# Kernel optimization log

Hardware: AMD Instinct MI355X
Metric: run time of the kernel (lower is better)

The kernel has to match this reference:

```python
import jax, jax.numpy as jnp
import numpy as np

B, D, LD, LP = 8, 192, 128, 1024
FC = [1024, 1024, 512]
NC = 2


def setup_inputs() -> dict:
    key = jax.random.key(0)
    ks = jax.random.split(key, 18)
    s = 0.05  # small init scale for numerical sanity
    inp = {
        "drug_conv": jax.random.normal(ks[0], (B, D, LD), jnp.float32),
        "protein_conv": jax.random.normal(ks[1], (B, D, LP), jnp.float32),
        "Wd": jax.random.normal(ks[2], (D, D), jnp.float32) * s,
        "bd": jax.random.normal(ks[3], (D,), jnp.float32) * s,
        "Wp": jax.random.normal(ks[4], (D, D), jnp.float32) * s,
        "bp": jax.random.normal(ks[5], (D,), jnp.float32) * s,
        "Wa": jax.random.normal(ks[6], (D, D), jnp.float32) * s,
        "ba": jax.random.normal(ks[7], (D,), jnp.float32) * s,
        "W1": jax.random.normal(ks[8], (FC[0], 2 * D), jnp.float32) * s,
        "b1": jax.random.normal(ks[9], (FC[0],), jnp.float32) * s,
        "W2": jax.random.normal(ks[10], (FC[1], FC[0]), jnp.float32) * s,
        "b2": jax.random.normal(ks[11], (FC[1],), jnp.float32) * s,
        "W3": jax.random.normal(ks[12], (FC[2], FC[1]), jnp.float32) * s,
        "b3": jax.random.normal(ks[13], (FC[2],), jnp.float32) * s,
        "Wo": jax.random.normal(ks[14], (NC, FC[2]), jnp.float32) * s,
        "bo": jax.random.normal(ks[15], (NC,), jnp.float32) * s,
    }
    return inp


def reference(drug_conv, protein_conv, Wd, bd, Wp, bp, Wa, ba,
              W1, b1, W2, b2, W3, b3, Wo, bo):
    # drug_conv: (B, D, Ld); protein_conv: (B, D, Lp). Torch Linear: y = x @ W.T + b
    d_att = jnp.einsum('bdl,ed->ble', drug_conv, Wd) + bd      # (B, Ld, D)
    p_att = jnp.einsum('bdl,ed->ble', protein_conv, Wp) + bp   # (B, Lp, D)
    # broadcast additive cross-attention: (B, Ld, Lp, D)
    h = jax.nn.relu(d_att[:, :, None, :] + p_att[:, None, :, :])
    A = jnp.einsum('blpd,ed->blpe', h, Wa) + ba                # (B, Ld, Lp, D)
    comp_att = jax.nn.sigmoid(jnp.mean(A, axis=2))             # (B, Ld, D)
    prot_att = jax.nn.sigmoid(jnp.mean(A, axis=1))             # (B, Lp, D)
    # gated residual: x*0.5 + x*att  (att permuted back to (B, D, L))
    drug = drug_conv * (0.5 + jnp.transpose(comp_att, (0, 2, 1)))
    prot = protein_conv * (0.5 + jnp.transpose(prot_att, (0, 2, 1)))
    # MaxPool1d over full sequence length == max along last axis
    drug_pooled = jnp.max(drug, axis=2)                        # (B, D)
    prot_pooled = jnp.max(prot, axis=2)                        # (B, D)
    pair = jnp.concatenate([drug_pooled, prot_pooled], axis=1) # (B, 2D)
    lrelu = lambda x: jax.nn.leaky_relu(x, 0.01)
    h1 = lrelu(pair @ W1.T + b1)
    h2 = lrelu(h1 @ W2.T + b2)
    h3 = lrelu(h2 @ W3.T + b3)
    return h3 @ Wo.T + bo                                      # (B, num_classes)
```

## Files before the change

### kernel.cpp

```cpp
#include <hip/hip_runtime.h>
#include <math.h>

#define BB 8
#define DD 192
#define LLD 128
#define LLP 1024
#define FC1 1024
#define FC2 1024
#define FC3 512
#define NCLS 2
#define LT 16

__global__ void proj_both_kernel(const float* __restrict__ drug,
                                 const float* __restrict__ prot,
                                 const float* __restrict__ Wd,
                                 const float* __restrict__ bdv,
                                 const float* __restrict__ Wp,
                                 const float* __restrict__ bpv,
                                 float* __restrict__ d_att,
                                 float* __restrict__ p_att) {
    int blk = blockIdx.x;
    const float *x, *W, *bias;
    float* y;
    int L, b, l0;
    if (blk < BB * (LLD / LT)) {
        x = drug; W = Wd; bias = bdv; y = d_att; L = LLD;
        b = blk >> 3; l0 = (blk & 7) * LT;
    } else {
        int idx = blk - BB * (LLD / LT);
        x = prot; W = Wp; bias = bpv; y = p_att; L = LLP;
        b = idx >> 6; l0 = (idx & 63) * LT;
    }
    int tid = threadIdx.x;

    __shared__ float xs[LT][DD + 4];

    const float* xbase = x + (size_t)b * DD * L + l0;
#pragma unroll
    for (int k = 0; k < LT; ++k) {
        int idx = tid + k * DD;
        int d = idx >> 4;
        int j = idx & (LT - 1);
        xs[j][d] = xbase[(size_t)d * L + j];
    }
    __syncthreads();

    const int e = tid;
    const float be = bias[e];
    float acc[LT];
#pragma unroll
    for (int j = 0; j < LT; ++j) acc[j] = be;

    const float4* Wr4 = (const float4*)(W + (size_t)e * DD);
#pragma unroll 2
    for (int d4 = 0; d4 < DD / 4; ++d4) {
        float4 w = Wr4[d4];
#pragma unroll
        for (int j = 0; j < LT; ++j) {
            float4 h = *(const float4*)&xs[j][d4 * 4];
            acc[j] = fmaf(h.x, w.x, acc[j]);
            acc[j] = fmaf(h.y, w.y, acc[j]);
            acc[j] = fmaf(h.z, w.z, acc[j]);
            acc[j] = fmaf(h.w, w.w, acc[j]);
        }
    }

    float* ybase = y + ((size_t)b * L + l0) * DD;
#pragma unroll
    for (int j = 0; j < LT; ++j)
        ybase[(size_t)j * DD + e] = acc[j];
}

__global__ void cross_sort_kernel(const float* __restrict__ da,
                                  const float* __restrict__ pa,
                                  float* __restrict__ Hd_t,
                                  float* __restrict__ Hp_t) {
    int blk = blockIdx.x;
    int b = blk / (DD / 2);
    int dp = blk - b * (DD / 2);
    int d0 = dp * 2;
    int tid = threadIdx.x;

    __shared__ float skey[2][LLD];
    __shared__ int   sidx[2][LLD];
    __shared__ float sufs[2][LLD + 1];
    __shared__ int   cnt[2][LLD + 1];
    __shared__ float val[2][LLD + 1];

    {
        int a = tid >> 7, l = tid & 127;
        skey[a][l] = da[((size_t)b * LLD + l) * DD + d0 + a];
        sidx[a][l] = l;
    }
    for (int i = tid; i < 2 * (LLD + 1); i += 256) {
        int a = i / (LLD + 1), k = i - a * (LLD + 1);
        cnt[a][k] = 0;
        val[a][k] = 0.f;
    }
    __syncthreads();

    {
        int a = tid >> 7, i = tid & 127;
        for (int k = 2; k <= LLD; k <<= 1) {
            for (int j = k >> 1; j > 0; j >>= 1) {
                int ixj = i ^ j;
                if (ixj > i) {
                    float ki = skey[a][i], kj = skey[a][ixj];
                    bool up = ((i & k) == 0);
                    if ((ki > kj) == up) {
                        skey[a][i] = kj; skey[a][ixj] = ki;
                        int t = sidx[a][i]; sidx[a][i] = sidx[a][ixj]; sidx[a][ixj] = t;
                    }
                }
                __syncthreads();
            }
        }
    }

    if (tid < 2) {
        float s = 0.f;
        sufs[tid][LLD] = 0.f;
        for (int r = LLD - 1; r >= 0; --r) {
            s += skey[tid][r];
            sufs[tid][r] = s;
        }
    }
    __syncthreads();

    {
        int d_i = tid & 1, prow = tid >> 1;
        float* hprow = Hp_t + ((size_t)b * DD + d0 + d_i) * LLP;
        const float* qbase = pa + (size_t)b * LLP * DD + d0 + d_i;
#pragma unroll
        for (int batch = 0; batch < LLP / 128; ++batch) {
            int p = batch * 128 + prow;
            float q = qbase[(size_t)p * DD];
            float nq = -q;
            int pos = 0;
#pragma unroll
            for (int st = LLD; st > 0; st >>= 1) {
                int np = pos + st;
                if (np <= LLD && skey[d_i][np - 1] <= nq) pos = np;
            }
            hprow[p] = ((float)(LLD - pos) * q + sufs[d_i][pos]) * (1.0f / LLD);
            atomicAdd(&cnt[d_i][pos], 1);
            atomicAdd(&val[d_i][pos], q);
        }
    }
    __syncthreads();

    if (tid < 2) {
        int c = 0; float v = 0.f;
        for (int k = 0; k < LLD; ++k) {
            c += cnt[tid][k]; cnt[tid][k] = c;
            v += val[tid][k]; val[tid][k] = v;
        }
    }
    __syncthreads();

    {
        int a = tid >> 7, r = tid & 127;
        float hv = (skey[a][r] * (float)cnt[a][r] + val[a][r]) * (1.0f / LLP);
        Hd_t[((size_t)b * DD + d0 + a) * LLD + sidx[a][r]] = hv;
    }
}

__global__ void gemm_sig_both_kernel(const float* __restrict__ Hd_t,
                                     const float* __restrict__ Hp_t,
                                     const float* __restrict__ Wa,
                                     const float* __restrict__ ba,
                                     float* __restrict__ catt_t,
                                     float* __restrict__ psig_t) {
    int blk = blockIdx.x;
    const float* Ht;
    float* out_t;
    int L, b, l0;
    if (blk < BB * (LLD / LT)) {
        b = blk >> 3; l0 = (blk & 7) * LT;
        Ht = Hd_t; out_t = catt_t; L = LLD;
    } else {
        int idx = blk - BB * (LLD / LT);
        b = idx >> 6; l0 = (idx & 63) * LT;
        Ht = Hp_t; out_t = psig_t; L = LLP;
    }
    int tid = threadIdx.x;

    __shared__ float hs[LT][DD];
    __shared__ float cs[LT][DD + 1];

    const float* hrow = Ht + ((size_t)b * DD + tid) * L + l0;
#pragma unroll
    for (int j = 0; j < LT; ++j) hs[j][tid] = hrow[j];
    __syncthreads();

    const int e = tid;
    const float bias = ba[e];
    float acc[LT];
#pragma unroll
    for (int j = 0; j < LT; ++j) acc[j] = bias;

    const float4* Wr4 = (const float4*)(Wa + (size_t)e * DD);
#pragma unroll 2
    for (int d4 = 0; d4 < DD / 4; ++d4) {
        float4 w = Wr4[d4];
#pragma unroll
        for (int j = 0; j < LT; ++j) {
            float4 h = *(const float4*)&hs[j][d4 * 4];
            acc[j] = fmaf(h.x, w.x, acc[j]);
            acc[j] = fmaf(h.y, w.y, acc[j]);
            acc[j] = fmaf(h.z, w.z, acc[j]);
            acc[j] = fmaf(h.w, w.w, acc[j]);
        }
    }

#pragma unroll
    for (int j = 0; j < LT; ++j)
        cs[j][e] = 1.0f / (1.0f + __expf(-acc[j]));
    __syncthreads();

    float* obase = out_t + (size_t)b * DD * L + l0;
    for (int k = tid; k < LT * DD; k += DD) {
        int eo = k >> 4;
        int j = k & (LT - 1);
        obase[(size_t)eo * L + j] = cs[j][eo];
    }
}

__global__ void pool_pair_kernel(const float* __restrict__ drug,
                                 const float* __restrict__ prot,
                                 const float* __restrict__ catt_t,
                                 const float* __restrict__ psig_t,
                                 float* __restrict__ pair) {
    int bd = blockIdx.x;
    int b = bd / DD;
    int d = bd - b * DD;
    int lane = threadIdx.x;

    const float* dr = drug + (size_t)bd * LLD;
    const float* ca = catt_t + (size_t)bd * LLD;
    float m1 = -INFINITY;
#pragma unroll
    for (int k = 0; k < LLD / 64; ++k) {
        int l = lane + 64 * k;
        m1 = fmaxf(m1, dr[l] * (0.5f + ca[l]));
    }

    const float* pr = prot + (size_t)bd * LLP;
    const float* ps = psig_t + (size_t)bd * LLP;
    float m2 = -INFINITY;
#pragma unroll
    for (int k = 0; k < LLP / 64; ++k) {
        int p = lane + 64 * k;
        m2 = fmaxf(m2, pr[p] * (0.5f + ps[p]));
    }

#pragma unroll
    for (int off = 32; off > 0; off >>= 1) {
        m1 = fmaxf(m1, __shfl_xor(m1, off));
        m2 = fmaxf(m2, __shfl_xor(m2, off));
    }
    if (lane == 0) {
        pair[b * 2 * DD + d] = m1;
        pair[b * 2 * DD + DD + d] = m2;
    }
}

__global__ void fc_wave_kernel(const float* __restrict__ x,
                               const float* __restrict__ W,
                               const float* __restrict__ bias,
                               float* __restrict__ y,
                               int K, int N, int leaky) {
    int gtid = blockIdx.x * blockDim.x + threadIdx.x;
    int wid = gtid >> 6;
    int lane = gtid & 63;
    if (wid >= BB * N) return;
    int b = wid / N;
    int j = wid - b * N;
    const float4* xr = (const float4*)(x + (size_t)b * K);
    const float4* Wr = (const float4*)(W + (size_t)j * K);
    int K4 = K >> 2;
    float s = 0.f;
    for (int k = lane; k < K4; k += 64) {
        float4 xv = xr[k];
        float4 wv = Wr[k];
        s = fmaf(xv.x, wv.x, s);
        s = fmaf(xv.y, wv.y, s);
        s = fmaf(xv.z, wv.z, s);
        s = fmaf(xv.w, wv.w, s);
    }
#pragma unroll
    for (int off = 32; off > 0; off >>= 1) s += __shfl_xor(s, off);
    if (lane == 0) {
        float acc = s + bias[j];
        if (leaky) acc = (acc > 0.f) ? acc : 0.01f * acc;
        y[wid] = acc;
    }
}

extern "C" void kernel_launch(void* const* d_in, const int* in_sizes, int n_in,
                              void* d_out, int out_size, void* d_ws, size_t ws_size,
                              hipStream_t stream) {
    const float* drug = (const float*)d_in[0];
    const float* prot = (const float*)d_in[1];
    const float* Wd = (const float*)d_in[2];
    const float* bd = (const float*)d_in[3];
    const float* Wp = (const float*)d_in[4];
    const float* bp = (const float*)d_in[5];
    const float* Wa = (const float*)d_in[6];
    const float* ba = (const float*)d_in[7];
    const float* W1 = (const float*)d_in[8];
    const float* b1 = (const float*)d_in[9];
    const float* W2 = (const float*)d_in[10];
    const float* b2 = (const float*)d_in[11];
    const float* W3 = (const float*)d_in[12];
    const float* b3 = (const float*)d_in[13];
    const float* Wo = (const float*)d_in[14];
    const float* bo = (const float*)d_in[15];
    float* out = (float*)d_out;

    float* ws = (float*)d_ws;
    const size_t n_datt = (size_t)BB * LLD * DD;
    const size_t n_patt = (size_t)BB * LLP * DD;
    float* d_att  = ws;
    float* p_att  = d_att + n_datt;
    float* Hd_t   = p_att + n_patt;
    float* Hp_t   = Hd_t + n_datt;
    float* catt_t = Hp_t + n_patt;
    float* psig_t = catt_t + n_datt;
    float* pair   = psig_t + n_patt;
    float* h1     = pair + (size_t)BB * 2 * DD;
    float* h2     = h1 + (size_t)BB * FC1;
    float* h3     = h2 + (size_t)BB * FC2;

    proj_both_kernel<<<BB * (LLD / LT) + BB * (LLP / LT), DD, 0, stream>>>(
        drug, prot, Wd, bd, Wp, bp, d_att, p_att);

    cross_sort_kernel<<<BB * (DD / 2), 256, 0, stream>>>(d_att, p_att, Hd_t, Hp_t);

    gemm_sig_both_kernel<<<BB * (LLD / LT) + BB * (LLP / LT), DD, 0, stream>>>(
        Hd_t, Hp_t, Wa, ba, catt_t, psig_t);

    pool_pair_kernel<<<BB * DD, 64, 0, stream>>>(drug, prot, catt_t, psig_t, pair);

    fc_wave_kernel<<<(BB * FC1 * 64) / 256, 256, 0, stream>>>(pair, W1, b1, h1, 2 * DD, FC1, 1);
    fc_wave_kernel<<<(BB * FC2 * 64) / 256, 256, 0, stream>>>(h1, W2, b2, h2, FC1, FC2, 1);
    fc_wave_kernel<<<(BB * FC3 * 64) / 256, 256, 0, stream>>>(h2, W3, b3, h3, FC2, FC3, 1);
    fc_wave_kernel<<<(BB * NCLS * 64 + 255) / 256, 256, 0, stream>>>(h3, Wo, bo, out, FC3, NCLS, 0);
}
```

Baseline: 110.0 us.

## Use 4x4 register tiles in projection GEMMs and parallel scans in sort kernel

Measured after the change: 153.3 us. +39.3%, slower.

```diff
diff --git a/kernel.cpp b/kernel.cpp
--- a/kernel.cpp
+++ b/kernel.cpp
@@ -45,30 +45,45 @@
     }
     __syncthreads();
 
-    const int e = tid;
-    const float be = bias[e];
-    float acc[LT];
-#pragma unroll
-    for (int j = 0; j < LT; ++j) acc[j] = be;
-
-    const float4* Wr4 = (const float4*)(W + (size_t)e * DD);
+    int et = tid % 48;
+    int lg = tid / 48;
+    int e0 = et * 4;
+    int jl0 = lg * 4;
+
+    float acc[4][4];
+#pragma unroll
+    for (int i = 0; i < 4; ++i) {
+        float be = bias[e0 + i];
+#pragma unroll
+        for (int j = 0; j < 4; ++j) acc[i][j] = be;
+    }
+
+    const float4* W4 = (const float4*)W;
 #pragma unroll 2
     for (int d4 = 0; d4 < DD / 4; ++d4) {
-        float4 w = Wr4[d4];
-#pragma unroll
-        for (int j = 0; j < LT; ++j) {
-            float4 h = *(const float4*)&xs[j][d4 * 4];
-            acc[j] = fmaf(h.x, w.x, acc[j]);
-            acc[j] = fmaf(h.y, w.y, acc[j]);
-            acc[j] = fmaf(h.z, w.z, acc[j]);
-            acc[j] = fmaf(h.w, w.w, acc[j]);
+        float4 h[4];
+#pragma unroll
+        for (int j = 0; j < 4; ++j)
+            h[j] = *(const float4*)&xs[jl0 + j][d4 * 4];
+#pragma unroll
+        for (int i = 0; i < 4; ++i) {
+            float4 w = W4[(size_t)(e0 + i) * (DD / 4) + d4];
+#pragma unroll
+            for (int j = 0; j < 4; ++j) {
+                acc[i][j] = fmaf(h[j].x, w.x, acc[i][j]);
+                acc[i][j] = fmaf(h[j].y, w.y, acc[i][j]);
+                acc[i][j] = fmaf(h[j].z, w.z, acc[i][j]);
+                acc[i][j] = fmaf(h[j].w, w.w, acc[i][j]);
+            }
         }
     }
 
     float* ybase = y + ((size_t)b * L + l0) * DD;
 #pragma unroll
-    for (int j = 0; j < LT; ++j)
-        ybase[(size_t)j * DD + e] = acc[j];
+    for (int j = 0; j < 4; ++j) {
+        float4 v = make_float4(acc[0][j], acc[1][j], acc[2][j], acc[3][j]);
+        *(float4*)&ybase[(size_t)(jl0 + j) * DD + e0] = v;
+    }
 }
 
 __global__ void cross_sort_kernel(const float* __restrict__ da,
@@ -97,6 +112,7 @@
         cnt[a][k] = 0;
         val[a][k] = 0.f;
     }
+    if (tid < 2) sufs[tid][LLD] = 0.f;
     __syncthreads();
 
     {
@@ -117,15 +133,17 @@
         }
     }
 
-    if (tid < 2) {
-        float s = 0.f;
-        sufs[tid][LLD] = 0.f;
-        for (int r = LLD - 1; r >= 0; --r) {
-            s += skey[tid][r];
-            sufs[tid][r] = s;
-        }
-    }
-    __syncthreads();
+    {
+        int a = tid >> 7, i = tid & 127;
+        sufs[a][i] = skey[a][i];
+        __syncthreads();
+        for (int off = 1; off < LLD; off <<= 1) {
+            float v = (i + off < LLD) ? sufs[a][i + off] : 0.f;
+            __syncthreads();
+            sufs[a][i] += v;
+            __syncthreads();
+        }
+    }
 
     {
         int d_i = tid & 1, prow = tid >> 1;
@@ -149,14 +167,17 @@
     }
     __syncthreads();
 
-    if (tid < 2) {
-        int c = 0; float v = 0.f;
-        for (int k = 0; k < LLD; ++k) {
-            c += cnt[tid][k]; cnt[tid][k] = c;
-            v += val[tid][k]; val[tid][k] = v;
-        }
-    }
-    __syncthreads();
+    {
+        int a = tid >> 7, i = tid & 127;
+        for (int off = 1; off < LLD; off <<= 1) {
+            int c = 0; float v = 0.f;
+            if (i >= off) { c = cnt[a][i - off]; v = val[a][i - off]; }
+            __syncthreads();
+            cnt[a][i] += c;
+            val[a][i] += v;
+            __syncthreads();
+        }
+    }
 
     {
         int a = tid >> 7, r = tid & 127;
@@ -185,7 +206,7 @@
     }
     int tid = threadIdx.x;
 
-    __shared__ float hs[LT][DD];
+    __shared__ float hs[LT][DD + 4];
     __shared__ float cs[LT][DD + 1];
 
     const float* hrow = Ht + ((size_t)b * DD + tid) * L + l0;
@@ -193,29 +214,44 @@
     for (int j = 0; j < LT; ++j) hs[j][tid] = hrow[j];
     __syncthreads();
 
-    const int e = tid;
-    const float bias = ba[e];
-    float acc[LT];
-#pragma unroll
-    for (int j = 0; j < LT; ++j) acc[j] = bias;
-
-    const float4* Wr4 = (const float4*)(Wa + (size_t)e * DD);
+    int et = tid % 48;
+    int lg = tid / 48;
+    int e0 = et * 4;
+    int jl0 = lg * 4;
+
+    float acc[4][4];
+#pragma unroll
+    for (int i = 0; i < 4; ++i) {
+        float be = ba[e0 + i];
+#pragma unroll
+        for (int j = 0; j < 4; ++j) acc[i][j] = be;
+    }
+
+    const float4* W4 = (const float4*)Wa;
 #pragma unroll 2
     for (int d4 = 0; d4 < DD / 4; ++d4) {
-        float4 w = Wr4[d4];
-#pragma unroll
-        for (int j = 0; j < LT; ++j) {
-            float4 h = *(const float4*)&hs[j][d4 * 4];
-            acc[j] = fmaf(h.x, w.x, acc[j]);
-            acc[j] = fmaf(h.y, w.y, acc[j]);
-            acc[j] = fmaf(h.z, w.z, acc[j]);
-            acc[j] = fmaf(h.w, w.w, acc[j]);
-        }
-    }
-
-#pragma unroll
-    for (int j = 0; j < LT; ++j)
-        cs[j][e] = 1.0f / (1.0f + __expf(-acc[j]));
+        float4 h[4];
+#pragma unroll
+        for (int j = 0; j < 4; ++j)
+            h[j] = *(const float4*)&hs[jl0 + j][d4 * 4];
+#pragma unroll
+        for (int i = 0; i < 4; ++i) {
+            float4 w = W4[(size_t)(e0 + i) * (DD / 4) + d4];
+#pragma unroll
+            for (int j = 0; j < 4; ++j) {
+                acc[i][j] = fmaf(h[j].x, w.x, acc[i][j]);
+                acc[i][j] = fmaf(h[j].y, w.y, acc[i][j]);
+                acc[i][j] = fmaf(h[j].z, w.z, acc[i][j]);
+                acc[i][j] = fmaf(h[j].w, w.w, acc[i][j]);
+            }
+        }
+    }
+
+#pragma unroll
+    for (int i = 0; i < 4; ++i)
+#pragma unroll
+        for (int j = 0; j < 4; ++j)
+            cs[jl0 + j][e0 + i] = 1.0f / (1.0f + __expf(-acc[i][j]));
     __syncthreads();
 
     float* obase = out_t + (size_t)b * DD * L + l0;
```
